# Performance work log

Hardware: AMD Instinct MI355X
Metric: run time of the kernel (lower is better)

Reference implementation:

```python
import jax, jax.numpy as jnp
import numpy as np

N_HEADS = 4
LEAKY_SLOPE = 0.2


def setup_inputs() -> dict:
    key = jax.random.key(0)
    k1, k2, k3 = jax.random.split(key, 3)
    b, c, h, w = 8, 64, 128, 128
    z = jax.random.normal(k1, (b, c, h, w), dtype=jnp.float32)
    # torch.nn.Linear weights are (out_features, in_features); scale ~1/sqrt(fan_in)
    W_Q = jax.random.normal(k2, (c, c), dtype=jnp.float32) * 0.125
    W_K = jax.random.normal(k3, (c, c), dtype=jnp.float32) * 0.125
    return {"z": z, "W_Q": W_Q, "W_K": W_K}


def _axial_branch(z_perm_flat, z_raw_flat, W_Q, W_K, n_batch, seq, d_k, scale):
    # z_perm_flat: (n_batch, seq, c)  -- rearranged input fed to W_Q
    # z_raw_flat : (n_batch, seq, c)  -- raw memory-order reshape fed to W_K
    Q = jnp.matmul(z_perm_flat, W_Q.T).reshape(N_HEADS * n_batch, d_k, seq)
    V = jnp.matmul(z_raw_flat, W_K.T).reshape(N_HEADS * n_batch, d_k, seq)
    # QK-less scores: Q^T Q / sqrt(d_k)  -> (N, seq, seq)
    scores = jnp.einsum('nds,ndt->nst', Q, Q) * scale
    attn = jax.nn.softmax(scores, axis=-1)
    # right-multiply attention onto V, then LeakyReLU
    ctx = jnp.einsum('nds,nst->ndt', V, attn)
    return jax.nn.leaky_relu(ctx, negative_slope=LEAKY_SLOPE)


def reference(z, W_Q, W_K):
    b, c, h, w = z.shape
    d_k = c // N_HEADS
    scale = 1.0 / np.sqrt(d_k).astype(np.float32)

    # Branch 1 (attention over w): a = rearrange 'b c h w -> (b h) w c'
    a = jnp.transpose(z, (0, 2, 3, 1)).reshape(b * h, w, c)
    v1_in = z.reshape(b * h, w, c)  # raw reshape, as in the torch code
    context1 = _axial_branch(a, v1_in, W_Q, W_K, b * h, w, d_k, scale)

    # Branch 2 (attention over h): m = rearrange 'b c h w -> (b w) h c'
    m = jnp.transpose(z, (0, 3, 2, 1)).reshape(b * w, h, c)
    v2_in = z.reshape(b * w, h, c)  # raw reshape, as in the torch code
    context2 = _axial_branch(m, v2_in, W_Q, W_K, b * w, h, d_k, scale)

    context = context1 + context2  # requires h == w
    return context.reshape(b, c, h, w)
```

## Files before the change

kernel.cpp:

```cpp
#include <hip/hip_runtime.h>


typedef __attribute__((ext_vector_type(8))) short bh8;
typedef __attribute__((ext_vector_type(4))) float f32x4;
typedef unsigned short u16;
typedef unsigned int u32;

#define MFMA16(a,b,c) __builtin_amdgcn_mfma_f32_16x16x32_bf16(a,b,c,0,0,0)

#define AIMG_ST 72
#define QP_ST   40
#define VH_ST   136
#define PT_ST   72

#define OFF_AH   0
#define OFF_AL   4608
#define OFF_VIN  9216
#define OFF_PT   0
#define OFF_QP   18432
#define OFF_VH   28672
#define LDS_TOT  33024

__device__ __forceinline__ void split3(float f, u16& h, u16& l) {
    u32 u = __float_as_uint(f);
    u32 hf = u & 0xFFFF0000u;
    float r = f - __uint_as_float(hf);
    h = (u16)(hf >> 16);
    l = (u16)((__float_as_uint(r) + 0x8000u) >> 16);
}
__device__ __forceinline__ u16 rnbf(float f) {
    return (u16)((__float_as_uint(f) + 0x8000u) >> 16);
}
__device__ __forceinline__ u32 pkrn(float f0, float f1) {
    return ((__float_as_uint(f0) + 0x8000u) >> 16) |
           ((__float_as_uint(f1) + 0x8000u) & 0xFFFF0000u);
}
__device__ __forceinline__ float lrelu(float x) { return x > 0.f ? x : 0.2f * x; }

__global__ void split_w_kernel(const float* __restrict__ Wq,
                               const float* __restrict__ Wk,
                               u16* __restrict__ ws)
{
    const int i = blockIdx.x * 256 + threadIdx.x;
    const int j = i & 4095;
    const float f = (i < 4096) ? Wq[j] : Wk[j];
    const int base = (i < 4096) ? 0 : 8192;
    u16 h, l; split3(f, h, l);
    ws[base + j] = h;
    ws[base + 4096 + j] = l;
}

#define WOFF(n, ks) (((n)*16 + lid)*64 + (ks)*32 + quad*8)

__device__ __forceinline__ void gemm_q(const u16* Ah, const u16* Al,
                                       const u16* wsu,
                                       u16* qp, int miQ, int niA, int lid, int quad)
{
    const bh8 h0a = *(const bh8*)(wsu +        WOFF(niA+0,0));
    const bh8 h0b = *(const bh8*)(wsu +        WOFF(niA+0,1));
    const bh8 h1a = *(const bh8*)(wsu +        WOFF(niA+1,0));
    const bh8 h1b = *(const bh8*)(wsu +        WOFF(niA+1,1));
    const bh8 l0a = *(const bh8*)(wsu + 4096 + WOFF(niA+0,0));
    const bh8 l0b = *(const bh8*)(wsu + 4096 + WOFF(niA+0,1));
    const bh8 l1a = *(const bh8*)(wsu + 4096 + WOFF(niA+1,0));
    const bh8 l1b = *(const bh8*)(wsu + 4096 + WOFF(niA+1,1));
    const int offA = (miQ*16 + lid)*AIMG_ST + quad*8;
    bh8 ah0 = *(const bh8*)(Ah + offA);
    bh8 ah1 = *(const bh8*)(Ah + offA + 32);
    bh8 al0 = *(const bh8*)(Al + offA);
    bh8 al1 = *(const bh8*)(Al + offA + 32);
    f32x4 acc0 = {0.f,0.f,0.f,0.f}, acc1 = {0.f,0.f,0.f,0.f};
    acc0 = MFMA16(ah0, h0a, acc0); acc0 = MFMA16(ah0, l0a, acc0); acc0 = MFMA16(al0, h0a, acc0);
    acc0 = MFMA16(ah1, h0b, acc0); acc0 = MFMA16(ah1, l0b, acc0); acc0 = MFMA16(al1, h0b, acc0);
    acc1 = MFMA16(ah0, h1a, acc1); acc1 = MFMA16(ah0, l1a, acc1); acc1 = MFMA16(al0, h1a, acc1);
    acc1 = MFMA16(ah1, h1b, acc1); acc1 = MFMA16(ah1, l1b, acc1); acc1 = MFMA16(al1, h1b, acc1);
    #pragma unroll
    for (int r = 0; r < 4; ++r) {
        const int l = miQ*16 + quad*4 + r;
        const int d = l >> 1;
        const int sbase = (l & 1) << 6;
        u16 h, lo;
        const int s0 = sbase + (niA + 0)*16 + lid;
        split3(0.5f*acc0[r], h, lo);
        qp[s0*QP_ST + d] = h; qp[s0*QP_ST + 16 + d] = lo;
        const int s1 = sbase + (niA + 1)*16 + lid;
        split3(0.5f*acc1[r], h, lo);
        qp[s1*QP_ST + d] = h; qp[s1*QP_ST + 16 + d] = lo;
    }
}

__device__ __forceinline__ void gemm_v(const u16* Vin, const u16* wsu,
                                       u16* vh, int miQ, int niA, int lid, int quad)
{
    const bh8 h0a = *(const bh8*)(wsu + 8192 + WOFF(niA+0,0));
    const bh8 h0b = *(const bh8*)(wsu + 8192 + WOFF(niA+0,1));
    const bh8 h1a = *(const bh8*)(wsu + 8192 + WOFF(niA+1,0));
    const bh8 h1b = *(const bh8*)(wsu + 8192 + WOFF(niA+1,1));
    const int offA = (miQ*16 + lid)*AIMG_ST + quad*8;
    bh8 ah0 = *(const bh8*)(Vin + offA);
    bh8 ah1 = *(const bh8*)(Vin + offA + 32);
    f32x4 acc0 = {0.f,0.f,0.f,0.f}, acc1 = {0.f,0.f,0.f,0.f};
    acc0 = MFMA16(ah0, h0a, acc0); acc0 = MFMA16(ah1, h0b, acc0);
    acc1 = MFMA16(ah0, h1a, acc1); acc1 = MFMA16(ah1, h1b, acc1);
    #pragma unroll
    for (int r = 0; r < 4; ++r) {
        const int l = miQ*16 + quad*4 + r;
        const int d = l >> 1;
        const int sbase = (l & 1) << 6;
        vh[d*VH_ST + sbase + (niA + 0)*16 + lid] = rnbf(acc0[r]);
        vh[d*VH_ST + sbase + (niA + 1)*16 + lid] = rnbf(acc1[r]);
    }
}

__device__ __forceinline__ void gram_pt(const u16* Qp, u16* PT, int h,
                                        int w, int lid, int quad)
{
    const u16* arow = Qp + (h*64 + 16*w + lid)*QP_ST;
    bh8 a1 = *(const bh8*)(arow + quad*8);
    bh8 t  = *(const bh8*)(arow + ((quad >= 2) ? (quad-2)*8 : 0));
    bh8 zz = t ^ t;
    bh8 a2 = (quad < 2) ? zz : t;
    f32x4 g[8];
    #pragma unroll
    for (int ti = 0; ti < 8; ++ti) {
        const u16* brow = Qp + (ti*16 + lid)*QP_ST;
        bh8 b1 = *(const bh8*)(brow + (quad & 1)*8);
        bh8 b2 = *(const bh8*)(brow + quad*8);
        f32x4 acc = {0.f,0.f,0.f,0.f};
        acc = MFMA16(a1, b1, acc);
        acc = MFMA16(a2, b2, acc);
        g[ti] = acc;
    }
    float inv[4];
    #pragma unroll
    for (int r = 0; r < 4; ++r) {
        float s = 0.f;
        #pragma unroll
        for (int ti = 0; ti < 8; ++ti) {
            const float p = __expf(g[ti][r]);
            g[ti][r] = p; s += p;
        }
        s += __shfl_xor(s, 1); s += __shfl_xor(s, 2);
        s += __shfl_xor(s, 4); s += __shfl_xor(s, 8);
        inv[r] = 1.0f / s;
    }
    const int col = 16*w + quad*4;
    #pragma unroll
    for (int ti = 0; ti < 8; ++ti) {
        uint2 dv;
        dv.x = pkrn(g[ti][0]*inv[0], g[ti][1]*inv[1]);
        dv.y = pkrn(g[ti][2]*inv[2], g[ti][3]*inv[3]);
        *(uint2*)(PT + (ti*16 + lid)*PT_ST + col) = dv;
    }
}

__device__ __forceinline__ void pv_ctx(const u16* PT, const u16* Vh, int h,
                                       f32x4& c0, f32x4& c1, int w, int lid, int quad)
{
    #pragma unroll
    for (int tj2 = 0; tj2 < 2; ++tj2) {
        const int tj = 2*w + tj2;
        f32x4 acc = tj2 ? c1 : c0;
        #pragma unroll
        for (int ks = 0; ks < 2; ++ks) {
            bh8 pa = *(const bh8*)(PT + (tj*16 + lid)*PT_ST + ks*32 + quad*8);
            bh8 vb = *(const bh8*)(Vh + lid*VH_ST + h*64 + ks*32 + quad*8);
            acc = MFMA16(pa, vb, acc);
        }
        if (tj2) c1 = acc; else c0 = acc;
    }
}

__global__ __launch_bounds__(256, 4)
void axial_attn_mfma(const float* __restrict__ z, const u16* __restrict__ wsu,
                     float* __restrict__ out)
{
    __shared__ __align__(16) unsigned char lds[LDS_TOT];
    u16* const ptAh = (u16*)(lds + OFF_AH);
    u16* const ptAl = (u16*)(lds + OFF_AL);
    u16* const ptPT = (u16*)(lds + OFF_PT);
    u16* const ptVI = (u16*)(lds + OFF_VIN);
    u16* const ptQP = (u16*)(lds + OFF_QP);
    u16* const ptVH = (u16*)(lds + OFF_VH);

    const int tid = threadIdx.x;
    const int w = tid >> 6, lane = tid & 63, quad = lane >> 4, lid = lane & 15;

    const int blk = blockIdx.x;
    const int j   = blk >> 3;
    const int xi  = ((blk & 7) << 4) | (j & 15);
    const int q   = (j >> 4) & 3;
    const int bi  = j >> 6;
    const int N   = (((bi << 7) | xi) << 2) | q;
    const size_t zbase = (size_t)bi << 20;

    const int ch0 = tid >> 5, l5 = tid & 31;
    const int vl0 = tid >> 4, vc0 = (tid & 15) << 2;
    const int miQ = w >> 1, niA = (w & 1) * 2;

    float a1r[8], a2r[8];
    float4 v4[2];
    {
        const float* s1 = z + zbase + ((size_t)xi << 7) + (q << 5) + l5;
        const float* s2 = z + zbase + (((size_t)(q*32 + l5)) << 7) + xi;
        #pragma unroll
        for (int k = 0; k < 8; ++k)
            a1r[k] = s1[(size_t)(ch0 + 8*k) << 14];
        const float4* sv = (const float4*)(z + ((size_t)N << 11));
        v4[0] = sv[tid]; v4[1] = sv[tid + 256];
        #pragma unroll
        for (int k = 0; k < 8; ++k)
            a2r[k] = s2[(size_t)(ch0 + 8*k) << 14];
    }

    #pragma unroll
    for (int k = 0; k < 8; ++k) {
        u16 h, lo; split3(a1r[k], h, lo);
        ptAh[l5*AIMG_ST + ch0 + 8*k] = h;
        ptAl[l5*AIMG_ST + ch0 + 8*k] = lo;
    }
    #pragma unroll
    for (int k = 0; k < 2; ++k) {
        const float4 vv = v4[k];
        uint2 dv;
        dv.x = pkrn(vv.x, vv.y);
        dv.y = pkrn(vv.z, vv.w);
        *(uint2*)(ptVI + (vl0 + 16*k)*AIMG_ST + vc0) = dv;
    }
    __syncthreads();

    gemm_q(ptAh, ptAl, wsu, ptQP, miQ, niA, lid, quad);
    gemm_v(ptVI, wsu, ptVH, miQ, niA, lid, quad);
    __syncthreads();

    f32x4 c10 = {0.f,0.f,0.f,0.f}, c11 = {0.f,0.f,0.f,0.f};
    gram_pt(ptQP, ptPT, 0, w, lid, quad);
    __syncthreads();
    pv_ctx(ptPT, ptVH, 0, c10, c11, w, lid, quad);
    __syncthreads();
    gram_pt(ptQP, ptPT, 1, w, lid, quad);
    __syncthreads();
    pv_ctx(ptPT, ptVH, 1, c10, c11, w, lid, quad);
    __syncthreads();

    #pragma unroll
    for (int k = 0; k < 8; ++k) {
        u16 h, lo; split3(a2r[k], h, lo);
        ptAh[l5*AIMG_ST + ch0 + 8*k] = h;
        ptAl[l5*AIMG_ST + ch0 + 8*k] = lo;
    }
    __syncthreads();

    gemm_q(ptAh, ptAl, wsu, ptQP, miQ, niA, lid, quad);
    __syncthreads();

    f32x4 c20 = {0.f,0.f,0.f,0.f}, c21 = {0.f,0.f,0.f,0.f};
    gram_pt(ptQP, ptPT, 0, w, lid, quad);
    __syncthreads();
    pv_ctx(ptPT, ptVH, 0, c20, c21, w, lid, quad);
    __syncthreads();
    gram_pt(ptQP, ptPT, 1, w, lid, quad);
    __syncthreads();
    pv_ctx(ptPT, ptVH, 1, c20, c21, w, lid, quad);

    float* ob = out + ((size_t)N << 11) + lid*128;
    #pragma unroll
    for (int tj2 = 0; tj2 < 2; ++tj2) {
        f32x4 a = tj2 ? c11 : c10;
        f32x4 b = tj2 ? c21 : c20;
        float4 ov;
        ov.x = lrelu(a[0]) + lrelu(b[0]);
        ov.y = lrelu(a[1]) + lrelu(b[1]);
        ov.z = lrelu(a[2]) + lrelu(b[2]);
        ov.w = lrelu(a[3]) + lrelu(b[3]);
        *(float4*)(ob + (2*w + tj2)*16 + quad*4) = ov;
    }
}

extern "C" void kernel_launch(void* const* d_in, const int* in_sizes, int n_in,
                              void* d_out, int out_size, void* d_ws, size_t ws_size,
                              hipStream_t stream) {
    const float* z  = (const float*)d_in[0];
    const float* Wq = (const float*)d_in[1];
    const float* Wk = (const float*)d_in[2];
    float* out = (float*)d_out;
    u16* ws = (u16*)d_ws;
    hipLaunchKernelGGL(split_w_kernel, dim3(32), dim3(256), 0, stream, Wq, Wk, ws);
    hipLaunchKernelGGL(axial_attn_mfma, dim3(4096), dim3(256), 0, stream, z, ws, out);
}
```

Baseline: 162.5 us.

## Fold softmax scale into W_Q, use exp2/rcp intrinsics and packed bf16 splits

Pre-scales W_Q by sqrt(0.5*log2(e)/sqrt(dk))-like constant so the Gram scores come out in log2 units, allowing raw exp2 instead of expf and dropping the 0.5 multiply. Replaces the division with hardware rcp and the manual rounding with packed bf16 conversion intrinsics. Rewrites the hi/lo split of input tiles to pack pairs and store 16-byte vectors to LDS by remapping thread-to-channel assignment. Trades some rounding differences (rcp approximation, low-part rounding) for fewer ALU ops and LDS stores.

Measured after the change: 156.9 us. -3.5%, faster.

```diff
diff --git a/kernel.cpp b/kernel.cpp
--- a/kernel.cpp
+++ b/kernel.cpp
@@ -21,6 +21,36 @@
 #define OFF_VH   28672
 #define LDS_TOT  33024
 
+__device__ __forceinline__ u32 cvtpk_rn(float f0, float f1) {
+#if __has_builtin(__builtin_amdgcn_cvt_pk_bf16_f32)
+    auto h = __builtin_amdgcn_cvt_pk_bf16_f32(f0, f1);
+    u32 r; __builtin_memcpy(&r, &h, sizeof(r)); return r;
+#else
+    return ((__float_as_uint(f0) + 0x8000u) >> 16) |
+           ((__float_as_uint(f1) + 0x8000u) & 0xFFFF0000u);
+#endif
+}
+__device__ __forceinline__ float fexp2(float x) {
+#if __has_builtin(__builtin_amdgcn_exp2f)
+    return __builtin_amdgcn_exp2f(x);
+#else
+    return exp2f(x);
+#endif
+}
+__device__ __forceinline__ float frcp(float x) {
+#if __has_builtin(__builtin_amdgcn_rcpf)
+    return __builtin_amdgcn_rcpf(x);
+#else
+    return 1.0f / x;
+#endif
+}
+__device__ __forceinline__ void splitpk(float f0, float f1, u32& hp, u32& lp) {
+    u32 u0 = __float_as_uint(f0), u1 = __float_as_uint(f1);
+    hp = __builtin_amdgcn_perm(u1, u0, 0x07060302u);
+    float r0 = f0 - __uint_as_float(u0 & 0xFFFF0000u);
+    float r1 = f1 - __uint_as_float(u1 & 0xFFFF0000u);
+    lp = cvtpk_rn(r0, r1);
+}
 __device__ __forceinline__ void split3(float f, u16& h, u16& l) {
     u32 u = __float_as_uint(f);
     u32 hf = u & 0xFFFF0000u;
@@ -31,10 +61,6 @@
 __device__ __forceinline__ u16 rnbf(float f) {
     return (u16)((__float_as_uint(f) + 0x8000u) >> 16);
 }
-__device__ __forceinline__ u32 pkrn(float f0, float f1) {
-    return ((__float_as_uint(f0) + 0x8000u) >> 16) |
-           ((__float_as_uint(f1) + 0x8000u) & 0xFFFF0000u);
-}
 __device__ __forceinline__ float lrelu(float x) { return x > 0.f ? x : 0.2f * x; }
 
 __global__ void split_w_kernel(const float* __restrict__ Wq,
@@ -43,7 +69,8 @@
 {
     const int i = blockIdx.x * 256 + threadIdx.x;
     const int j = i & 4095;
-    const float f = (i < 4096) ? Wq[j] : Wk[j];
+    const float scale = (i < 4096) ? 0.6005612043932249f : 1.0f;
+    const float f = ((i < 4096) ? Wq[j] : Wk[j]) * scale;
     const int base = (i < 4096) ? 0 : 8192;
     u16 h, l; split3(f, h, l);
     ws[base + j] = h;
@@ -79,13 +106,14 @@
         const int l = miQ*16 + quad*4 + r;
         const int d = l >> 1;
         const int sbase = (l & 1) << 6;
-        u16 h, lo;
         const int s0 = sbase + (niA + 0)*16 + lid;
-        split3(0.5f*acc0[r], h, lo);
-        qp[s0*QP_ST + d] = h; qp[s0*QP_ST + 16 + d] = lo;
         const int s1 = sbase + (niA + 1)*16 + lid;
-        split3(0.5f*acc1[r], h, lo);
-        qp[s1*QP_ST + d] = h; qp[s1*QP_ST + 16 + d] = lo;
+        u32 hp, lp;
+        splitpk(acc0[r], acc1[r], hp, lp);
+        qp[s0*QP_ST + d]      = (u16)hp;
+        qp[s0*QP_ST + 16 + d] = (u16)lp;
+        qp[s1*QP_ST + d]      = (u16)(hp >> 16);
+        qp[s1*QP_ST + 16 + d] = (u16)(lp >> 16);
     }
 }
 
@@ -137,19 +165,19 @@
         float s = 0.f;
         #pragma unroll
         for (int ti = 0; ti < 8; ++ti) {
-            const float p = __expf(g[ti][r]);
+            const float p = fexp2(g[ti][r]);
             g[ti][r] = p; s += p;
         }
         s += __shfl_xor(s, 1); s += __shfl_xor(s, 2);
         s += __shfl_xor(s, 4); s += __shfl_xor(s, 8);
-        inv[r] = 1.0f / s;
+        inv[r] = frcp(s);
     }
     const int col = 16*w + quad*4;
     #pragma unroll
     for (int ti = 0; ti < 8; ++ti) {
         uint2 dv;
-        dv.x = pkrn(g[ti][0]*inv[0], g[ti][1]*inv[1]);
-        dv.y = pkrn(g[ti][2]*inv[2], g[ti][3]*inv[3]);
+        dv.x = cvtpk_rn(g[ti][0]*inv[0], g[ti][1]*inv[1]);
+        dv.y = cvtpk_rn(g[ti][2]*inv[2], g[ti][3]*inv[3]);
         *(uint2*)(PT + (ti*16 + lid)*PT_ST + col) = dv;
     }
 }
@@ -194,7 +222,7 @@
     const int N   = (((bi << 7) | xi) << 2) | q;
     const size_t zbase = (size_t)bi << 20;
 
-    const int ch0 = tid >> 5, l5 = tid & 31;
+    const int c8 = tid >> 5, l5 = tid & 31;
     const int vl0 = tid >> 4, vc0 = (tid & 15) << 2;
     const int miQ = w >> 1, niA = (w & 1) * 2;
 
@@ -205,26 +233,27 @@
         const float* s2 = z + zbase + (((size_t)(q*32 + l5)) << 7) + xi;
         #pragma unroll
         for (int k = 0; k < 8; ++k)
-            a1r[k] = s1[(size_t)(ch0 + 8*k) << 14];
+            a1r[k] = s1[(size_t)(c8*8 + k) << 14];
         const float4* sv = (const float4*)(z + ((size_t)N << 11));
         v4[0] = sv[tid]; v4[1] = sv[tid + 256];
         #pragma unroll
         for (int k = 0; k < 8; ++k)
-            a2r[k] = s2[(size_t)(ch0 + 8*k) << 14];
-    }
-
-    #pragma unroll
-    for (int k = 0; k < 8; ++k) {
-        u16 h, lo; split3(a1r[k], h, lo);
-        ptAh[l5*AIMG_ST + ch0 + 8*k] = h;
-        ptAl[l5*AIMG_ST + ch0 + 8*k] = lo;
+            a2r[k] = s2[(size_t)(c8*8 + k) << 14];
+    }
+
+    {
+        u32 hp[4], lp[4];
+        #pragma unroll
+        for (int k = 0; k < 4; ++k) splitpk(a1r[2*k], a1r[2*k+1], hp[k], lp[k]);
+        *(uint4*)(ptAh + l5*AIMG_ST + c8*8) = make_uint4(hp[0], hp[1], hp[2], hp[3]);
+        *(uint4*)(ptAl + l5*AIMG_ST + c8*8) = make_uint4(lp[0], lp[1], lp[2], lp[3]);
     }
     #pragma unroll
     for (int k = 0; k < 2; ++k) {
         const float4 vv = v4[k];
         uint2 dv;
-        dv.x = pkrn(vv.x, vv.y);
-        dv.y = pkrn(vv.z, vv.w);
+        dv.x = cvtpk_rn(vv.x, vv.y);
+        dv.y = cvtpk_rn(vv.z, vv.w);
         *(uint2*)(ptVI + (vl0 + 16*k)*AIMG_ST + vc0) = dv;
     }
     __syncthreads();
@@ -243,11 +272,12 @@
     pv_ctx(ptPT, ptVH, 1, c10, c11, w, lid, quad);
     __syncthreads();
 
-    #pragma unroll
-    for (int k = 0; k < 8; ++k) {
-        u16 h, lo; split3(a2r[k], h, lo);
-        ptAh[l5*AIMG_ST + ch0 + 8*k] = h;
-        ptAl[l5*AIMG_ST + ch0 + 8*k] = lo;
+    {
+        u32 hp[4], lp[4];
+        #pragma unroll
+        for (int k = 0; k < 4; ++k) splitpk(a2r[2*k], a2r[2*k+1], hp[k], lp[k]);
+        *(uint4*)(ptAh + l5*AIMG_ST + c8*8) = make_uint4(hp[0], hp[1], hp[2], hp[3]);
+        *(uint4*)(ptAl + l5*AIMG_ST + c8*8) = make_uint4(lp[0], lp[1], lp[2], lp[3]);
     }
     __syncthreads();
 
```
